# Kernel tuning notes

Hardware: AMD Instinct MI355X
Metric: run time of the kernel (lower is better)

Reference implementation:

```python
import jax, jax.numpy as jnp
import numpy as np

N_NODES = 100000
N_EDGES = 1600000
IN_F = 128
OUT_F = 64
K = 2


def _propagate(x, src, dst, num_nodes):
    """GCN propagation with self-loops already appended to (src, dst).
    out[j] = sum_{(i->j)} deg(i)^-1/2 * deg(j)^-1/2 * x[i]
    where deg is the in-degree counting self-loops (PyG gcn_norm)."""
    deg = jnp.zeros((num_nodes,), dtype=x.dtype).at[dst].add(1.0)
    dinv = jnp.where(deg > 0, jax.lax.rsqrt(deg), 0.0)
    norm = dinv[src] * dinv[dst]                      # [E+N]
    msg = x[src] * norm[:, None]                      # gather + scale
    return jnp.zeros_like(x).at[dst].add(msg)         # scatter-add


def setup_inputs() -> dict:
    key = jax.random.key(0)
    k1, k2, k3, k4 = jax.random.split(key, 4)
    x = jax.random.normal(k1, (N_NODES, IN_F), dtype=jnp.float32)
    edge_index = jax.random.randint(k2, (2, N_EDGES), 0, N_NODES, dtype=jnp.int64)
    # Linear weights, torch convention: y = x @ W.T, W is [out, in]
    W1 = jax.random.normal(k3, (IN_F, IN_F), dtype=jnp.float32) / np.sqrt(IN_F)
    W2 = jax.random.normal(k4, (OUT_F, IN_F), dtype=jnp.float32) / np.sqrt(IN_F)
    return {"x": x, "edge_index": edge_index, "W1": W1, "W2": W2}


def reference(x, edge_index, W1, W2):
    num_nodes = x.shape[0]
    # add self loops once (same augmented edge set used by P1 and P2)
    loop = jnp.arange(num_nodes, dtype=edge_index.dtype)
    src = jnp.concatenate([edge_index[0], loop])
    dst = jnp.concatenate([edge_index[1], loop])
    for _ in range(K):
        x = x @ W1.T
        x = _propagate(x, src, dst, num_nodes)
    x = x @ W2.T
    x = _propagate(x, src, dst, num_nodes)
    # original computes log_softmax into `out` but returns pre-softmax x
    return x
```

## Files before the change

kernel.cpp:

```cpp
#include <hip/hip_runtime.h>

#define NN 100000
#define NE 1600000
#define ENT (NE + NN)
#define NB 196
#define BINCAP 10240


__global__ void probe_zero(const unsigned* __restrict__ edges, int* __restrict__ flag,
                           int* __restrict__ binCnt) {
    int t = threadIdx.x;
    if (t < NB) binCnt[t] = 0;
    if (t == 0) {
        int is64 = 1;
        for (int i = 1; i < 64; i += 2)
            if (edges[i] != 0u) { is64 = 0; break; }
        *flag = is64;
    }
}


__global__ __launch_bounds__(256) void part_kernel(const void* __restrict__ edges,
                                                   const int* __restrict__ flag,
                                                   int* __restrict__ binned,
                                                   int* __restrict__ binCnt) {
    __shared__ int hist[NB], base[NB], rank[NB];
    int t = threadIdx.x;
    for (int i = t; i < NB; i += 256) hist[i] = 0;
    __syncthreads();
    int i0 = blockIdx.x * 4096;
    bool is64 = (*flag != 0);
    int s[16], d[16];
    #pragma unroll
    for (int q = 0; q < 16; ++q) {
        int i = i0 + q * 256 + t;
        if (i < NE) {
            if (is64) {
                s[q] = (int)__builtin_nontemporal_load(&((const long long*)edges)[i]);
                d[q] = (int)__builtin_nontemporal_load(&((const long long*)edges)[NE + i]);
            } else {
                s[q] = __builtin_nontemporal_load(&((const int*)edges)[i]);
                d[q] = __builtin_nontemporal_load(&((const int*)edges)[NE + i]);
            }
            atomicAdd(&hist[d[q] >> 9], 1);
        } else d[q] = -1;
    }
    __syncthreads();
    for (int i = t; i < NB; i += 256) {
        base[i] = atomicAdd(&binCnt[i], hist[i]);
        rank[i] = 0;
    }
    __syncthreads();
    #pragma unroll
    for (int q = 0; q < 16; ++q) {
        if (d[q] >= 0) {
            int b = d[q] >> 9;
            int r = base[b] + atomicAdd(&rank[b], 1);
            if (r < BINCAP)
                binned[(size_t)b * BINCAP + r] = ((d[q] & 511) << 17) | s[q];
        }
    }
}


__global__ __launch_bounds__(1024) void build2_kernel(const int* __restrict__ binCnt,
                                                      const int* __restrict__ binned,
                                                      float* __restrict__ dinv,
                                                      int* __restrict__ rowoff,
                                                      int* __restrict__ edge) {
    extern __shared__ char smem[];
    int* stage = (int*)smem;
    int* hist  = (int*)(smem + (size_t)BINCAP * 4);
    int* sc    = hist + 512;
    int* cur   = sc + 512;
    int* bsc   = cur + 512;
    int b = blockIdx.x, t = threadIdx.x;
    int nb0 = b << 9;
    int nNodes = min(512, NN - nb0);

    if (t < 256) {
        int nodes = (t < NB) ? min(512, NN - (t << 9)) : 0;
        bsc[t] = (t < NB) ? binCnt[t] + nodes : 0;
    }
    if (t < 512) hist[t] = 0;
    __syncthreads();
    for (int off = 1; off < 256; off <<= 1) {
        int a = (t < 256 && t >= off) ? bsc[t - off] : 0;
        __syncthreads();
        if (t < 256) bsc[t] += a;
        __syncthreads();
    }
    int cntRaw = binCnt[b];
    int cnt = min(cntRaw, BINCAP);
    int off0 = bsc[b] - (cntRaw + nNodes);

    const int* e = binned + (size_t)b * BINCAP;
    for (int i = t; i < cnt; i += 1024) atomicAdd(&hist[e[i] >> 17], 1);
    __syncthreads();
    int v = 0;
    if (t < 512) { v = (t < nNodes) ? hist[t] + 1 : 0; sc[t] = v; }
    __syncthreads();
    for (int off = 1; off < 512; off <<= 1) {
        int a = (t < 512 && t >= off) ? sc[t - off] : 0;
        __syncthreads();
        if (t < 512) sc[t] += a;
        __syncthreads();
    }
    if (t < nNodes) {
        dinv[nb0 + t] = rsqrtf((float)(hist[t] + 1));
        int lo = sc[t] - v;
        rowoff[nb0 + t] = off0 + lo;
        stage[lo] = nb0 + t;
        cur[t] = lo + 1;
    }
    if (b == NB - 1 && t == 0) rowoff[NN] = ENT;
    __syncthreads();
    for (int i = t; i < cnt; i += 1024) {
        int pk = e[i];
        int slot = atomicAdd(&cur[pk >> 17], 1);
        if (slot < BINCAP) stage[slot] = pk & 0x1FFFF;
    }
    __syncthreads();
    int total = min(cntRaw + nNodes, BINCAP);
    int* dst = edge + off0;
    for (int i = t; i < total; i += 1024) dst[i] = stage[i];
}


__global__ __launch_bounds__(256) void wprod1_kernel(const float* __restrict__ W1,
                                                     const float* __restrict__ W2,
                                                     float* __restrict__ T) {
    int idx = blockIdx.x * blockDim.x + threadIdx.x;
    if (idx >= 128 * 64) return;
    int k = idx >> 6, j = idx & 63;
    float s = 0.f;
    #pragma unroll 8
    for (int q = 0; q < 128; ++q)
        s += W1[q * 128 + k] * W2[j * 128 + q];
    T[k * 64 + j] = s;
}

__global__ __launch_bounds__(256) void wprod2_kernel(const float* __restrict__ W1,
                                                     const float* __restrict__ T,
                                                     float* __restrict__ WcT) {
    int idx = blockIdx.x * blockDim.x + threadIdx.x;
    if (idx >= 128 * 64) return;
    int i = idx >> 6, j = idx & 63;
    float s = 0.f;
    #pragma unroll 8
    for (int k = 0; k < 128; ++k)
        s += W1[k * 128 + i] * T[k * 64 + j];
    WcT[j * 128 + i] = s;
}


template<int SPOW>
__global__ __launch_bounds__(256) void spmm64f_kernel(const int* __restrict__ rowoff,
                                                      const int* __restrict__ col,
                                                      const float* __restrict__ dinv,
                                                      const float* __restrict__ H,
                                                      float* __restrict__ O) {
    int w = (int)((blockIdx.x * (unsigned)blockDim.x + threadIdx.x) >> 6);
    if (w >= NN) return;
    int lane = threadIdx.x & 63;
    int s = __builtin_amdgcn_readfirstlane(rowoff[w]);
    int e = __builtin_amdgcn_readfirstlane(rowoff[w + 1]);
    float acc = 0.f;
    const float* base = H + lane;

    int p = s;
    for (; p + 8 <= e; p += 8) {
        int c[8];
        #pragma unroll
        for (int q = 0; q < 8; ++q) c[q] = __builtin_nontemporal_load(&col[p + q]);
        #pragma unroll
        for (int q = 0; q < 8; ++q) acc += base[(size_t)c[q] * 64];
    }
    if (p + 4 <= e) {
        int c[4];
        #pragma unroll
        for (int q = 0; q < 4; ++q) c[q] = __builtin_nontemporal_load(&col[p + q]);
        #pragma unroll
        for (int q = 0; q < 4; ++q) acc += base[(size_t)c[q] * 64];
        p += 4;
    }
    for (; p < e; ++p) acc += base[(size_t)__builtin_nontemporal_load(&col[p]) * 64];

    float di = dinv[w];
    float scale = (SPOW == 2) ? di * di : di;
    __builtin_nontemporal_store(acc * scale, &O[(size_t)w * 64 + lane]);
}


__global__ __launch_bounds__(256) void gemm_xwt64_kernel(const float* __restrict__ X,
                                                         const float* __restrict__ W,
                                                         const float* __restrict__ dinv,
                                                         float* __restrict__ Y, int M) {
    constexpr int N = 64, K = 128, BM = 64, BK = 32;
    constexpr int TM = 4, TN = N / 16;
    __shared__ float Xs[BK][BM + 4];
    __shared__ float Ws[BK][N + 4];
    int t  = threadIdx.x;
    int m0 = blockIdx.x * BM;
    int r0 = (t >> 4) * TM;
    int c0 = (t & 15) * TN;
    float acc[TM][TN] = {};
    for (int k0 = 0; k0 < K; k0 += BK) {
        #pragma unroll
        for (int i = 0; i < 2; ++i) {
            int f  = t + i * 256;
            int m  = f >> 3;
            int kq = (f & 7) << 2;
            int gm = m0 + m; if (gm >= M) gm = M - 1;
            float4 v = *(const float4*)&X[(size_t)gm * K + k0 + kq];
            Xs[kq + 0][m] = v.x; Xs[kq + 1][m] = v.y;
            Xs[kq + 2][m] = v.z; Xs[kq + 3][m] = v.w;
        }
        #pragma unroll
        for (int i = 0; i < N / 32; ++i) {
            int f  = t + i * 256;
            int n  = f >> 3;
            int kq = (f & 7) << 2;
            float4 v = *(const float4*)&W[(size_t)n * K + k0 + kq];
            Ws[kq + 0][n] = v.x; Ws[kq + 1][n] = v.y;
            Ws[kq + 2][n] = v.z; Ws[kq + 3][n] = v.w;
        }
        __syncthreads();
        #pragma unroll
        for (int k = 0; k < BK; ++k) {
            float4 xv = *(const float4*)&Xs[k][r0];
            float xf[TM] = {xv.x, xv.y, xv.z, xv.w};
            float wf[TN];
            #pragma unroll
            for (int j = 0; j < TN; j += 4) {
                float4 wv = *(const float4*)&Ws[k][c0 + j];
                wf[j] = wv.x; wf[j + 1] = wv.y; wf[j + 2] = wv.z; wf[j + 3] = wv.w;
            }
            #pragma unroll
            for (int i = 0; i < TM; ++i)
                #pragma unroll
                for (int j = 0; j < TN; ++j)
                    acc[i][j] += xf[i] * wf[j];
        }
        __syncthreads();
    }
    #pragma unroll
    for (int i = 0; i < TM; ++i) {
        int gm = m0 + r0 + i;
        if (gm < M) {
            float di = dinv[gm];
            #pragma unroll
            for (int j = 0; j < TN; j += 4) {
                float4 v = {di * acc[i][j], di * acc[i][j + 1],
                            di * acc[i][j + 2], di * acc[i][j + 3]};
                *(float4*)&Y[(size_t)gm * N + c0 + j] = v;
            }
        }
    }
}


extern "C" void kernel_launch(void* const* d_in, const int* in_sizes, int n_in,
                              void* d_out, int out_size, void* d_ws, size_t ws_size,
                              hipStream_t stream) {
    const float* x     = (const float*)d_in[0];
    const void*  edges = d_in[1];
    const float* W1    = (const float*)d_in[2];
    const float* W2    = (const float*)d_in[3];
    float* out = (float*)d_out;

    char* ws = (char*)d_ws;
    size_t off = 0;
    auto take = [&](size_t bytes) -> char* {
        char* p = ws + off;
        off = (off + bytes + 255) & ~(size_t)255;
        return p;
    };
    int*   flag   = (int*)take(4);
    int*   binCnt = (int*)take((size_t)NB * 4);
    float* dinv   = (float*)take((size_t)NN * 4);
    int*   rowoff = (int*)take((size_t)(NN + 1) * 4);
    float* Tbuf   = (float*)take((size_t)128 * 64 * 4);
    float* WcT    = (float*)take((size_t)64 * 128 * 4);
    int*   binned = (int*)take((size_t)NB * BINCAP * 4);
    int*   edgeA  = (int*)take((size_t)ENT * 4);
    float* g      = (float*)take((size_t)NN * 64 * 4);
    float* y      = (float*)take((size_t)NN * 64 * 4);
    if (off > ws_size) return;

    probe_zero<<<1, 256, 0, stream>>>((const unsigned*)edges, flag, binCnt);
    wprod1_kernel<<<32, 256, 0, stream>>>(W1, W2, Tbuf);
    wprod2_kernel<<<32, 256, 0, stream>>>(W1, Tbuf, WcT);
    part_kernel<<<(NE + 4095) / 4096, 256, 0, stream>>>(edges, flag, binned, binCnt);
    size_t b2lds = (size_t)BINCAP * 4 + (512 * 3 + 256) * 4;
    build2_kernel<<<NB, 1024, b2lds, stream>>>(binCnt, binned, dinv, rowoff, edgeA);

    const int GB = (NN + 63) / 64;
    const int PB = (NN * 64 + 255) / 256;

    gemm_xwt64_kernel<<<GB, 256, 0, stream>>>(x, WcT, dinv, g, NN);
    spmm64f_kernel<2><<<PB, 256, 0, stream>>>(rowoff, edgeA, dinv, g, y);
    spmm64f_kernel<2><<<PB, 256, 0, stream>>>(rowoff, edgeA, dinv, y, g);
    spmm64f_kernel<1><<<PB, 256, 0, stream>>>(rowoff, edgeA, dinv, g, out);
}
```

Baseline: 262.8 us.

## Split SpMM rows across feature halves and edge parity; fold probe into wprod1

The SpMM kernel now gives each 64-lane wave one node and one 32-feature half. The two 32-lane halves of the wave take alternating edges and combine their sums with a cross-lane shuffle. The grid doubles to 50000 blocks, and a block-ID mapping places both feature halves of the same nodes in nearby blocks, aiming for more memory-level parallelism and a shorter serial edge chain per wave. The probe/zero kernel is folded into wprod1 to save one launch. The cost is a shuffle per node, half the lanes idle at the store, and each row's offsets and column indices are read twice.

New measurement: 419.7 us. +59.7%, slower.

```diff
diff --git a/kernel.cpp b/kernel.cpp
--- a/kernel.cpp
+++ b/kernel.cpp
@@ -5,19 +5,6 @@
 #define ENT (NE + NN)
 #define NB 196
 #define BINCAP 10240
-
-
-__global__ void probe_zero(const unsigned* __restrict__ edges, int* __restrict__ flag,
-                           int* __restrict__ binCnt) {
-    int t = threadIdx.x;
-    if (t < NB) binCnt[t] = 0;
-    if (t == 0) {
-        int is64 = 1;
-        for (int i = 1; i < 64; i += 2)
-            if (edges[i] != 0u) { is64 = 0; break; }
-        *flag = is64;
-    }
-}
 
 
 __global__ __launch_bounds__(256) void part_kernel(const void* __restrict__ edges,
@@ -129,7 +116,20 @@
 
 __global__ __launch_bounds__(256) void wprod1_kernel(const float* __restrict__ W1,
                                                      const float* __restrict__ W2,
-                                                     float* __restrict__ T) {
+                                                     float* __restrict__ T,
+                                                     const unsigned* __restrict__ edges,
+                                                     int* __restrict__ flag,
+                                                     int* __restrict__ binCnt) {
+    if (blockIdx.x == 0) {
+        int t = threadIdx.x;
+        if (t < NB) binCnt[t] = 0;
+        if (t == 0) {
+            int is64 = 1;
+            for (int i = 1; i < 64; i += 2)
+                if (edges[i] != 0u) { is64 = 0; break; }
+            *flag = is64;
+        }
+    }
     int idx = blockIdx.x * blockDim.x + threadIdx.x;
     if (idx >= 128 * 64) return;
     int k = idx >> 6, j = idx & 63;
@@ -155,40 +155,55 @@
 
 
 template<int SPOW>
-__global__ __launch_bounds__(256) void spmm64f_kernel(const int* __restrict__ rowoff,
-                                                      const int* __restrict__ col,
-                                                      const float* __restrict__ dinv,
-                                                      const float* __restrict__ H,
-                                                      float* __restrict__ O) {
-    int w = (int)((blockIdx.x * (unsigned)blockDim.x + threadIdx.x) >> 6);
+__global__ __launch_bounds__(256) void spmm32_kernel(const int* __restrict__ rowoff,
+                                                     const int* __restrict__ col,
+                                                     const float* __restrict__ dinv,
+                                                     const float* __restrict__ H,
+                                                     float* __restrict__ O) {
+    int bid = blockIdx.x;
+    int u = bid >> 3, x = bid & 7;
+    int half = x >> 2;
+    int nodeblk = u * 4 + (x & 3);
+    int w = nodeblk * 4 + (threadIdx.x >> 6);
     if (w >= NN) return;
     int lane = threadIdx.x & 63;
+    int hw = lane >> 5;
+    int fl = lane & 31;
     int s = __builtin_amdgcn_readfirstlane(rowoff[w]);
     int e = __builtin_amdgcn_readfirstlane(rowoff[w + 1]);
+    const float* base = H + half * 32 + fl;
     float acc = 0.f;
-    const float* base = H + lane;
-
     int p = s;
     for (; p + 8 <= e; p += 8) {
-        int c[8];
-        #pragma unroll
-        for (int q = 0; q < 8; ++q) c[q] = __builtin_nontemporal_load(&col[p + q]);
-        #pragma unroll
-        for (int q = 0; q < 8; ++q) acc += base[(size_t)c[q] * 64];
+        int c[4];
+        #pragma unroll
+        for (int q = 0; q < 4; ++q)
+            c[q] = __builtin_nontemporal_load(&col[p + 2 * q + hw]);
+        #pragma unroll
+        for (int q = 0; q < 4; ++q)
+            acc += base[(size_t)c[q] * 64];
     }
     if (p + 4 <= e) {
-        int c[4];
-        #pragma unroll
-        for (int q = 0; q < 4; ++q) c[q] = __builtin_nontemporal_load(&col[p + q]);
-        #pragma unroll
-        for (int q = 0; q < 4; ++q) acc += base[(size_t)c[q] * 64];
+        int c[2];
+        #pragma unroll
+        for (int q = 0; q < 2; ++q)
+            c[q] = __builtin_nontemporal_load(&col[p + 2 * q + hw]);
+        #pragma unroll
+        for (int q = 0; q < 2; ++q)
+            acc += base[(size_t)c[q] * 64];
         p += 4;
     }
-    for (; p < e; ++p) acc += base[(size_t)__builtin_nontemporal_load(&col[p]) * 64];
-
-    float di = dinv[w];
-    float scale = (SPOW == 2) ? di * di : di;
-    __builtin_nontemporal_store(acc * scale, &O[(size_t)w * 64 + lane]);
+    for (; p < e; p += 2) {
+        int idx = p + hw;
+        if (idx < e)
+            acc += base[(size_t)__builtin_nontemporal_load(&col[idx]) * 64];
+    }
+    acc += __shfl_xor(acc, 32, 64);
+    if (hw == 0) {
+        float di = dinv[w];
+        float sc = (SPOW == 2) ? di * di : di;
+        __builtin_nontemporal_store(acc * sc, &O[(size_t)w * 64 + half * 32 + fl]);
+    }
 }
 
 
@@ -288,18 +303,17 @@
     float* y      = (float*)take((size_t)NN * 64 * 4);
     if (off > ws_size) return;
 
-    probe_zero<<<1, 256, 0, stream>>>((const unsigned*)edges, flag, binCnt);
-    wprod1_kernel<<<32, 256, 0, stream>>>(W1, W2, Tbuf);
+    wprod1_kernel<<<32, 256, 0, stream>>>(W1, W2, Tbuf, (const unsigned*)edges, flag, binCnt);
     wprod2_kernel<<<32, 256, 0, stream>>>(W1, Tbuf, WcT);
     part_kernel<<<(NE + 4095) / 4096, 256, 0, stream>>>(edges, flag, binned, binCnt);
     size_t b2lds = (size_t)BINCAP * 4 + (512 * 3 + 256) * 4;
     build2_kernel<<<NB, 1024, b2lds, stream>>>(binCnt, binned, dinv, rowoff, edgeA);
 
     const int GB = (NN + 63) / 64;
-    const int PB = (NN * 64 + 255) / 256;
+    const int SB = 50000;
 
     gemm_xwt64_kernel<<<GB, 256, 0, stream>>>(x, WcT, dinv, g, NN);
-    spmm64f_kernel<2><<<PB, 256, 0, stream>>>(rowoff, edgeA, dinv, g, y);
-    spmm64f_kernel<2><<<PB, 256, 0, stream>>>(rowoff, edgeA, dinv, y, g);
-    spmm64f_kernel<1><<<PB, 256, 0, stream>>>(rowoff, edgeA, dinv, g, out);
-}
+    spmm32_kernel<2><<<SB, 256, 0, stream>>>(rowoff, edgeA, dinv, g, y);
+    spmm32_kernel<2><<<SB, 256, 0, stream>>>(rowoff, edgeA, dinv, y, g);
+    spmm32_kernel<1><<<SB, 256, 0, stream>>>(rowoff, edgeA, dinv, g, out);
+}
```
